# Performance work log

Hardware: AMD Instinct MI355X
Metric: run time of the kernel (lower is better)

Reference implementation:

```python
import jax, jax.numpy as jnp
import numpy as np

VOCAB = 50000
DIM = 20      # vector_dim; must equal RNN hidden size per the classifier shape constraint
HID = 20
NCLS = 5
B, S = 16384, 256

def setup_inputs() -> dict:
    key = jax.random.key(0)
    k1, k2, k3, k4, k5, k6 = jax.random.split(key, 6)
    x = jax.random.randint(k1, (B, S), 0, VOCAB, dtype=jnp.int64)
    emb = jax.random.normal(k2, (VOCAB, DIM), dtype=jnp.float32)
    W_ih = jax.random.normal(k3, (HID, DIM), dtype=jnp.float32) * 0.1
    W_hh = jax.random.normal(k4, (HID, HID), dtype=jnp.float32) * 0.1
    W_cls = jax.random.normal(k5, (NCLS, DIM), dtype=jnp.float32) * 0.1
    b_cls = jax.random.normal(k6, (NCLS,), dtype=jnp.float32) * 0.1
    return {"x": x, "emb": emb, "W_ih": W_ih, "W_hh": W_hh, "W_cls": W_cls, "b_cls": b_cls}

def reference(x, emb, W_ih, W_hh, W_cls, b_cls):
    # padding_idx=0: row 0 of embedding is zero
    emb = emb.at[0].set(0.0)
    xe = emb[x]                                   # [B, S, DIM]
    # precompute input projection for all timesteps in one big matmul
    xp = jnp.einsum('bsd,hd->sbh', xe, W_ih)      # [S, B, HID]
    h0 = jnp.zeros((x.shape[0], HID), dtype=xe.dtype)

    def step(h, xt):
        h = jnp.tanh(xt + h @ W_hh.T)
        return h, None

    h_last, _ = jax.lax.scan(step, h0, xp)        # [B, HID]
    y_pred = h_last @ W_cls.T + b_cls             # [B, 5]
    return y_pred
```

## Files before the change

kernel.cpp:

```cpp
#include <hip/hip_runtime.h>
#include <hip/hip_bf16.h>

#define SEQ  256
#define DIM  20
#define NCLS 5

typedef short  bf16x8 __attribute__((ext_vector_type(8)));
typedef float  f32x4  __attribute__((ext_vector_type(4)));
typedef float  v2f    __attribute__((ext_vector_type(2)));

__device__ __forceinline__ v2f fast_tanh2(v2f x) {
    v2f xs = x * 2.8853900817779268f;
    v2f e;
    e.x = __builtin_amdgcn_exp2f(xs.x);
    e.y = __builtin_amdgcn_exp2f(xs.y);
    v2f d = e + 1.0f;
    v2f r;
    r.x = __builtin_amdgcn_rcpf(d.x);
    r.y = __builtin_amdgcn_rcpf(d.y);
    return __builtin_elementwise_fma((v2f)(-2.0f), r, (v2f)(1.0f));
}

__device__ __forceinline__ int cvt_pk_bf16(float lo, float hi) {
    int r;
    asm("v_cvt_pk_bf16_f32 %0, %1, %2" : "=v"(r) : "v"(lo), "v"(hi));
    return r;
}

__device__ __forceinline__ void pl32swap(int &a, int &b) {
    asm("v_permlane32_swap_b32 %0, %1" : "+v"(a), "+v"(b));
}

__device__ __forceinline__ int permk(int k) {
    return (k >= 4 && k < 8) ? k + 4 : (k >= 8 && k < 12) ? k - 4 : k;
}

union I4B { int i[4]; bf16x8 f; };

__global__ __launch_bounds__(256)
__attribute__((amdgpu_waves_per_eu(1, 1)))
void rnn_mfma(const int* __restrict__ x,
              const float* __restrict__ emb,
              const float* __restrict__ W_ih,
              const float* __restrict__ W_hh,
              const float* __restrict__ W_cls,
              const float* __restrict__ b_cls,
              float* __restrict__ out, int B)
{
    const int gtid = blockIdx.x * blockDim.x + threadIdx.x;
    const int wave = gtid >> 6;
    const int lane = (int)(threadIdx.x & 63);
    const int c = lane & 15;
    const int q = lane >> 4;
    const int row0 = wave * 16;
    if (row0 >= B) return;

    auto loadA = [&](const float* M, int U0, int ROWS, bool pk) {
        bf16x8 f;
        const int uu = U0 + c;
        const int ur = uu < ROWS ? uu : 0;
#pragma unroll
        for (int j = 0; j < 8; ++j) {
            const int kk = 8 * q + j;
            const int kp = pk ? permk(kk) : kk;
            const int kr = kp < DIM ? kp : 0;
            float v = M[ur * DIM + kr];
            v = (uu < ROWS && kk < DIM) ? v : 0.0f;
            __hip_bfloat16 hb = __float2bfloat16(v);
            f[j] = *reinterpret_cast<short*>(&hb);
        }
        return f;
    };
    const bf16x8 A0h = loadA(W_hh,  0, DIM,  true);
    const bf16x8 A0e = loadA(W_ih,  0, DIM,  false);
    const bf16x8 A1h = loadA(W_hh, 16, DIM,  true);
    const bf16x8 A1e = loadA(W_ih, 16, DIM,  false);
    const bf16x8 Acl = loadA(W_cls, 0, NCLS, true);

    float bias[4];
#pragma unroll
    for (int j = 0; j < 4; ++j) {
        const int idx = 4 * q + j;
        bias[j] = (idx < NCLS) ? b_cls[idx] : 0.0f;
    }

    const int eoff0 = (q == 0) ? 0 : (q == 1) ? 8 : 16;
    const int eoff1 = (q == 0) ? 4 : (q == 1) ? 12 : 16;

    const int* xp = x + (size_t)(row0 + c) * SEQ;
    const f32x4 zf = {0.0f, 0.0f, 0.0f, 0.0f};

    I4B Bh; Bh.i[0] = Bh.i[1] = Bh.i[2] = Bh.i[3] = 0;
    I4B Be;
    const int tk0 = xp[0];
    const int tk1 = xp[1];
    const int tk2 = xp[2];
    {
        const f32x4 lo = *(const f32x4*)(emb + (size_t)tk0 * DIM + eoff0);
        const f32x4 hi = *(const f32x4*)(emb + (size_t)tk0 * DIM + eoff1);
        const bool nz = (tk0 != 0);
        Be.i[0] = nz ? cvt_pk_bf16(lo[0], lo[1]) : 0;
        Be.i[1] = nz ? cvt_pk_bf16(lo[2], lo[3]) : 0;
        Be.i[2] = nz ? cvt_pk_bf16(hi[0], hi[1]) : 0;
        Be.i[3] = nz ? cvt_pk_bf16(hi[2], hi[3]) : 0;
    }
    f32x4 aePre0 = __builtin_amdgcn_mfma_f32_16x16x32_bf16(A0e, Be.f, zf, 0, 0, 0);
    f32x4 aePre1 = __builtin_amdgcn_mfma_f32_16x16x32_bf16(A1e, Be.f, zf, 0, 0, 0);

    f32x4 loA, hiA, loB, hiB;
    bool nzA, nzB;
    loA = *(const f32x4*)(emb + (size_t)tk1 * DIM + eoff0);
    hiA = *(const f32x4*)(emb + (size_t)tk1 * DIM + eoff1);
    nzA = (tk1 != 0);
    loB = *(const f32x4*)(emb + (size_t)tk2 * DIM + eoff0);
    hiB = *(const f32x4*)(emb + (size_t)tk2 * DIM + eoff1);
    nzB = (tk2 != 0);
    int tokG  = xp[3];
    int tokG2 = xp[4];

#pragma unroll 4
    for (int s = 0; s < SEQ; ++s) {
        const f32x4 loC = *(const f32x4*)(emb + (size_t)tokG * DIM + eoff0);
        const f32x4 hiC = *(const f32x4*)(emb + (size_t)tokG * DIM + eoff1);
        const bool nzC = (tokG != 0);
        const int i5 = (s + 5 < SEQ) ? (s + 5) : (SEQ - 1);
        const int tokNew = xp[i5];

        const f32x4 acc0 = __builtin_amdgcn_mfma_f32_16x16x32_bf16(A0h, Bh.f, aePre0, 0, 0, 0);
        const f32x4 acc1 = __builtin_amdgcn_mfma_f32_16x16x32_bf16(A1h, Bh.f, aePre1, 0, 0, 0);

        const v2f p0 = fast_tanh2((v2f){acc0[0], acc0[1]});
        const v2f p1 = fast_tanh2((v2f){acc0[2], acc0[3]});
        const v2f p2 = fast_tanh2((v2f){acc1[0], acc1[1]});
        const v2f p3 = fast_tanh2((v2f){acc1[2], acc1[3]});
        int w0  = cvt_pk_bf16(p0.x, p0.y);
        int w1  = cvt_pk_bf16(p1.x, p1.y);
        int tp0 = cvt_pk_bf16(p2.x, p2.y);
        int tp1 = cvt_pk_bf16(p3.x, p3.y);
        pl32swap(w0, tp0);
        pl32swap(w1, tp1);
        Bh.i[0] = w0;
        Bh.i[1] = w1;
        Bh.i[2] = tp0;
        Bh.i[3] = tp1;

        Be.i[0] = nzA ? cvt_pk_bf16(loA[0], loA[1]) : 0;
        Be.i[1] = nzA ? cvt_pk_bf16(loA[2], loA[3]) : 0;
        Be.i[2] = nzA ? cvt_pk_bf16(hiA[0], hiA[1]) : 0;
        Be.i[3] = nzA ? cvt_pk_bf16(hiA[2], hiA[3]) : 0;

        aePre0 = __builtin_amdgcn_mfma_f32_16x16x32_bf16(A0e, Be.f, zf, 0, 0, 0);
        aePre1 = __builtin_amdgcn_mfma_f32_16x16x32_bf16(A1e, Be.f, zf, 0, 0, 0);

        loA = loB; hiA = hiB; nzA = nzB;
        loB = loC; hiB = hiC; nzB = nzC;
        tokG = tokG2; tokG2 = tokNew;
    }

    const f32x4 y = __builtin_amdgcn_mfma_f32_16x16x32_bf16(Acl, Bh.f, zf, 0, 0, 0);
    float* orow = out + (size_t)(row0 + c) * NCLS;
    if (q == 0) {
        orow[0] = y[0] + bias[0];
        orow[1] = y[1] + bias[1];
        orow[2] = y[2] + bias[2];
        orow[3] = y[3] + bias[3];
    } else if (q == 1) {
        orow[4] = y[0] + bias[0];
    }
}

extern "C" void kernel_launch(void* const* d_in, const int* in_sizes, int n_in,
                              void* d_out, int out_size, void* d_ws, size_t ws_size,
                              hipStream_t stream) {
    const int*   x     = (const int*)d_in[0];
    const float* emb   = (const float*)d_in[1];
    const float* W_ih  = (const float*)d_in[2];
    const float* W_hh  = (const float*)d_in[3];
    const float* W_cls = (const float*)d_in[4];
    const float* b_cls = (const float*)d_in[5];
    float* out = (float*)d_out;

    const int B = in_sizes[0] / SEQ;
    const int threads = B * 4;
    const int block = 256;
    const int grid = (threads + block - 1) / block;
    rnn_mfma<<<grid, block, 0, stream>>>(x, emb, W_ih, W_hh, W_cls, b_cls, out, B);
}
```

Baseline: 74.74 us.

## Pre-convert embedding table to padded bf16 rows in workspace for single-load gathers

Adds a pre-pass kernel that converts the fp32 embedding table into a bf16 table padded to 32 entries per row, with the padding row and tail columns already zeroed. The RNN kernel then gathers each timestep's B-operand with one 16-byte load, with no per-step conversion or zero-token masking. This halves gather bytes and removes ALU work in the recurrence loop. In exchange, every call pays an extra launch and a full-table conversion pass (about 3 MB written), and falls back to the old kernel when workspace is too small.

```diff
diff --git a/kernel.cpp b/kernel.cpp
--- a/kernel.cpp
+++ b/kernel.cpp
@@ -4,6 +4,7 @@
 #define SEQ  256
 #define DIM  20
 #define NCLS 5
+#define VROW 32
 
 typedef short  bf16x8 __attribute__((ext_vector_type(8)));
 typedef float  f32x4  __attribute__((ext_vector_type(4)));
@@ -37,15 +38,29 @@
 
 union I4B { int i[4]; bf16x8 f; };
 
+__global__ void build_embB(const float* __restrict__ emb,
+                           unsigned short* __restrict__ embB, int V)
+{
+    int i = blockIdx.x * blockDim.x + threadIdx.x;
+    const int N = V * VROW;
+    const int stride = gridDim.x * blockDim.x;
+    for (; i < N; i += stride) {
+        const int tok = i >> 5, k = i & 31;
+        float v = (k < DIM && tok != 0) ? emb[tok * DIM + k] : 0.0f;
+        __hip_bfloat16 hb = __float2bfloat16(v);
+        embB[i] = *reinterpret_cast<unsigned short*>(&hb);
+    }
+}
+
 __global__ __launch_bounds__(256)
 __attribute__((amdgpu_waves_per_eu(1, 1)))
-void rnn_mfma(const int* __restrict__ x,
-              const float* __restrict__ emb,
-              const float* __restrict__ W_ih,
-              const float* __restrict__ W_hh,
-              const float* __restrict__ W_cls,
-              const float* __restrict__ b_cls,
-              float* __restrict__ out, int B)
+void rnn_mfma_tab(const int* __restrict__ x,
+                  const unsigned short* __restrict__ embB,
+                  const float* __restrict__ W_ih,
+                  const float* __restrict__ W_hh,
+                  const float* __restrict__ W_cls,
+                  const float* __restrict__ b_cls,
+                  float* __restrict__ out, int B)
 {
     const int gtid = blockIdx.x * blockDim.x + threadIdx.x;
     const int wave = gtid >> 6;
@@ -84,45 +99,29 @@
         bias[j] = (idx < NCLS) ? b_cls[idx] : 0.0f;
     }
 
-    const int eoff0 = (q == 0) ? 0 : (q == 1) ? 8 : 16;
-    const int eoff1 = (q == 0) ? 4 : (q == 1) ? 12 : 16;
-
     const int* xp = x + (size_t)(row0 + c) * SEQ;
     const f32x4 zf = {0.0f, 0.0f, 0.0f, 0.0f};
+    const unsigned short* ebq = embB + q * 8;
 
     I4B Bh; Bh.i[0] = Bh.i[1] = Bh.i[2] = Bh.i[3] = 0;
-    I4B Be;
     const int tk0 = xp[0];
     const int tk1 = xp[1];
     const int tk2 = xp[2];
-    {
-        const f32x4 lo = *(const f32x4*)(emb + (size_t)tk0 * DIM + eoff0);
-        const f32x4 hi = *(const f32x4*)(emb + (size_t)tk0 * DIM + eoff1);
-        const bool nz = (tk0 != 0);
-        Be.i[0] = nz ? cvt_pk_bf16(lo[0], lo[1]) : 0;
-        Be.i[1] = nz ? cvt_pk_bf16(lo[2], lo[3]) : 0;
-        Be.i[2] = nz ? cvt_pk_bf16(hi[0], hi[1]) : 0;
-        Be.i[3] = nz ? cvt_pk_bf16(hi[2], hi[3]) : 0;
-    }
-    f32x4 aePre0 = __builtin_amdgcn_mfma_f32_16x16x32_bf16(A0e, Be.f, zf, 0, 0, 0);
-    f32x4 aePre1 = __builtin_amdgcn_mfma_f32_16x16x32_bf16(A1e, Be.f, zf, 0, 0, 0);
-
-    f32x4 loA, hiA, loB, hiB;
-    bool nzA, nzB;
-    loA = *(const f32x4*)(emb + (size_t)tk1 * DIM + eoff0);
-    hiA = *(const f32x4*)(emb + (size_t)tk1 * DIM + eoff1);
-    nzA = (tk1 != 0);
-    loB = *(const f32x4*)(emb + (size_t)tk2 * DIM + eoff0);
-    hiB = *(const f32x4*)(emb + (size_t)tk2 * DIM + eoff1);
-    nzB = (tk2 != 0);
+    I4B Be0;
+    Be0.f = *(const bf16x8*)(ebq + (size_t)tk0 * VROW);
+    f32x4 aePre0 = __builtin_amdgcn_mfma_f32_16x16x32_bf16(A0e, Be0.f, zf, 0, 0, 0);
+    f32x4 aePre1 = __builtin_amdgcn_mfma_f32_16x16x32_bf16(A1e, Be0.f, zf, 0, 0, 0);
+
+    I4B gA, gB;
+    gA.f = *(const bf16x8*)(ebq + (size_t)tk1 * VROW);
+    gB.f = *(const bf16x8*)(ebq + (size_t)tk2 * VROW);
     int tokG  = xp[3];
     int tokG2 = xp[4];
 
 #pragma unroll 4
     for (int s = 0; s < SEQ; ++s) {
-        const f32x4 loC = *(const f32x4*)(emb + (size_t)tokG * DIM + eoff0);
-        const f32x4 hiC = *(const f32x4*)(emb + (size_t)tokG * DIM + eoff1);
-        const bool nzC = (tokG != 0);
+        I4B gC;
+        gC.f = *(const bf16x8*)(ebq + (size_t)tokG * VROW);
         const int i5 = (s + 5 < SEQ) ? (s + 5) : (SEQ - 1);
         const int tokNew = xp[i5];
 
@@ -144,6 +143,132 @@
         Bh.i[2] = tp0;
         Bh.i[3] = tp1;
 
+        aePre0 = __builtin_amdgcn_mfma_f32_16x16x32_bf16(A0e, gA.f, zf, 0, 0, 0);
+        aePre1 = __builtin_amdgcn_mfma_f32_16x16x32_bf16(A1e, gA.f, zf, 0, 0, 0);
+
+        gA = gB; gB = gC;
+        tokG = tokG2; tokG2 = tokNew;
+    }
+
+    const f32x4 y = __builtin_amdgcn_mfma_f32_16x16x32_bf16(Acl, Bh.f, zf, 0, 0, 0);
+    float* orow = out + (size_t)(row0 + c) * NCLS;
+    if (q == 0) {
+        orow[0] = y[0] + bias[0];
+        orow[1] = y[1] + bias[1];
+        orow[2] = y[2] + bias[2];
+        orow[3] = y[3] + bias[3];
+    } else if (q == 1) {
+        orow[4] = y[0] + bias[0];
+    }
+}
+
+__global__ __launch_bounds__(256)
+__attribute__((amdgpu_waves_per_eu(1, 1)))
+void rnn_mfma_fb(const int* __restrict__ x,
+                 const float* __restrict__ emb,
+                 const float* __restrict__ W_ih,
+                 const float* __restrict__ W_hh,
+                 const float* __restrict__ W_cls,
+                 const float* __restrict__ b_cls,
+                 float* __restrict__ out, int B)
+{
+    const int gtid = blockIdx.x * blockDim.x + threadIdx.x;
+    const int wave = gtid >> 6;
+    const int lane = (int)(threadIdx.x & 63);
+    const int c = lane & 15;
+    const int q = lane >> 4;
+    const int row0 = wave * 16;
+    if (row0 >= B) return;
+
+    auto loadA = [&](const float* M, int U0, int ROWS, bool pk) {
+        bf16x8 f;
+        const int uu = U0 + c;
+        const int ur = uu < ROWS ? uu : 0;
+#pragma unroll
+        for (int j = 0; j < 8; ++j) {
+            const int kk = 8 * q + j;
+            const int kp = pk ? permk(kk) : kk;
+            const int kr = kp < DIM ? kp : 0;
+            float v = M[ur * DIM + kr];
+            v = (uu < ROWS && kk < DIM) ? v : 0.0f;
+            __hip_bfloat16 hb = __float2bfloat16(v);
+            f[j] = *reinterpret_cast<short*>(&hb);
+        }
+        return f;
+    };
+    const bf16x8 A0h = loadA(W_hh,  0, DIM,  true);
+    const bf16x8 A0e = loadA(W_ih,  0, DIM,  false);
+    const bf16x8 A1h = loadA(W_hh, 16, DIM,  true);
+    const bf16x8 A1e = loadA(W_ih, 16, DIM,  false);
+    const bf16x8 Acl = loadA(W_cls, 0, NCLS, true);
+
+    float bias[4];
+#pragma unroll
+    for (int j = 0; j < 4; ++j) {
+        const int idx = 4 * q + j;
+        bias[j] = (idx < NCLS) ? b_cls[idx] : 0.0f;
+    }
+
+    const int eoff0 = (q == 0) ? 0 : (q == 1) ? 8 : 16;
+    const int eoff1 = (q == 0) ? 4 : (q == 1) ? 12 : 16;
+
+    const int* xp = x + (size_t)(row0 + c) * SEQ;
+    const f32x4 zf = {0.0f, 0.0f, 0.0f, 0.0f};
+
+    I4B Bh; Bh.i[0] = Bh.i[1] = Bh.i[2] = Bh.i[3] = 0;
+    I4B Be;
+    const int tk0 = xp[0];
+    const int tk1 = xp[1];
+    const int tk2 = xp[2];
+    {
+        const f32x4 lo = *(const f32x4*)(emb + (size_t)tk0 * DIM + eoff0);
+        const f32x4 hi = *(const f32x4*)(emb + (size_t)tk0 * DIM + eoff1);
+        const bool nz = (tk0 != 0);
+        Be.i[0] = nz ? cvt_pk_bf16(lo[0], lo[1]) : 0;
+        Be.i[1] = nz ? cvt_pk_bf16(lo[2], lo[3]) : 0;
+        Be.i[2] = nz ? cvt_pk_bf16(hi[0], hi[1]) : 0;
+        Be.i[3] = nz ? cvt_pk_bf16(hi[2], hi[3]) : 0;
+    }
+    f32x4 aePre0 = __builtin_amdgcn_mfma_f32_16x16x32_bf16(A0e, Be.f, zf, 0, 0, 0);
+    f32x4 aePre1 = __builtin_amdgcn_mfma_f32_16x16x32_bf16(A1e, Be.f, zf, 0, 0, 0);
+
+    f32x4 loA, hiA, loB, hiB;
+    bool nzA, nzB;
+    loA = *(const f32x4*)(emb + (size_t)tk1 * DIM + eoff0);
+    hiA = *(const f32x4*)(emb + (size_t)tk1 * DIM + eoff1);
+    nzA = (tk1 != 0);
+    loB = *(const f32x4*)(emb + (size_t)tk2 * DIM + eoff0);
+    hiB = *(const f32x4*)(emb + (size_t)tk2 * DIM + eoff1);
+    nzB = (tk2 != 0);
+    int tokG  = xp[3];
+    int tokG2 = xp[4];
+
+#pragma unroll 4
+    for (int s = 0; s < SEQ; ++s) {
+        const f32x4 loC = *(const f32x4*)(emb + (size_t)tokG * DIM + eoff0);
+        const f32x4 hiC = *(const f32x4*)(emb + (size_t)tokG * DIM + eoff1);
+        const bool nzC = (tokG != 0);
+        const int i5 = (s + 5 < SEQ) ? (s + 5) : (SEQ - 1);
+        const int tokNew = xp[i5];
+
+        const f32x4 acc0 = __builtin_amdgcn_mfma_f32_16x16x32_bf16(A0h, Bh.f, aePre0, 0, 0, 0);
+        const f32x4 acc1 = __builtin_amdgcn_mfma_f32_16x16x32_bf16(A1h, Bh.f, aePre1, 0, 0, 0);
+
+        const v2f p0 = fast_tanh2((v2f){acc0[0], acc0[1]});
+        const v2f p1 = fast_tanh2((v2f){acc0[2], acc0[3]});
+        const v2f p2 = fast_tanh2((v2f){acc1[0], acc1[1]});
+        const v2f p3 = fast_tanh2((v2f){acc1[2], acc1[3]});
+        int w0  = cvt_pk_bf16(p0.x, p0.y);
+        int w1  = cvt_pk_bf16(p1.x, p1.y);
+        int tp0 = cvt_pk_bf16(p2.x, p2.y);
+        int tp1 = cvt_pk_bf16(p3.x, p3.y);
+        pl32swap(w0, tp0);
+        pl32swap(w1, tp1);
+        Bh.i[0] = w0;
+        Bh.i[1] = w1;
+        Bh.i[2] = tp0;
+        Bh.i[3] = tp1;
+
         Be.i[0] = nzA ? cvt_pk_bf16(loA[0], loA[1]) : 0;
         Be.i[1] = nzA ? cvt_pk_bf16(loA[2], loA[3]) : 0;
         Be.i[2] = nzA ? cvt_pk_bf16(hiA[0], hiA[1]) : 0;
@@ -181,8 +306,18 @@
     float* out = (float*)d_out;
 
     const int B = in_sizes[0] / SEQ;
+    const int V = in_sizes[1] / DIM;
+    const size_t tabBytes = (size_t)V * VROW * sizeof(unsigned short);
+
     const int threads = B * 4;
     const int block = 256;
     const int grid = (threads + block - 1) / block;
-    rnn_mfma<<<grid, block, 0, stream>>>(x, emb, W_ih, W_hh, W_cls, b_cls, out, B);
-}
+
+    if (d_ws != nullptr && ws_size >= tabBytes) {
+        unsigned short* embB = (unsigned short*)d_ws;
+        build_embB<<<1024, 256, 0, stream>>>(emb, embB, V);
+        rnn_mfma_tab<<<grid, block, 0, stream>>>(x, embB, W_ih, W_hh, W_cls, b_cls, out, B);
+    } else {
+        rnn_mfma_fb<<<grid, block, 0, stream>>>(x, emb, W_ih, W_hh, W_cls, b_cls, out, B);
+    }
+}
```

Result: slower. 91.66 us (+22.6%).
